# Kernel optimization log

Hardware: AMD Instinct MI355X
Metric: run time of the kernel (lower is better)

The kernel has to match this reference:

```python
import jax, jax.numpy as jnp
import numpy as np

N = 6
DT = 0.02
EPS = 1e-6
_R, _C = np.tril_indices(N)  # row-major lower-triangle order, matches the torch double loop


def _mlp(x, W1, b1, W2, b2, W3, b3):
    h = jax.nn.softplus(x @ W1 + b1)
    h = jax.nn.softplus(h @ W2 + b2)
    return h @ W3 + b3


def _trig(q):
    # interleaved [cos q0, sin q0, cos q1, sin q1, ...]
    return jnp.stack([jnp.cos(q), jnp.sin(q)], axis=-1).reshape(q.shape[:-1] + (2 * N,))


def _mass_single(q, pL):
    # q: (6,) -> M: (6,6)
    y = _mlp(_trig(q), *pL)  # (21,)
    L = jnp.zeros((N, N), y.dtype).at[_R, _C].set(y)
    return L @ L.T + EPS * jnp.eye(N, dtype=y.dtype)


def _mass_batched(q, pL):
    y = _mlp(_trig(q), *pL)  # (B,21)
    L = jnp.zeros((q.shape[0], N, N), y.dtype).at[:, _R, _C].set(y)
    return jnp.einsum('bik,bjk->bij', L, L) + EPS * jnp.eye(N, dtype=y.dtype)


def _pot_batched(q, pV):
    return _mlp(_trig(q), *pV)[:, 0]  # (B,)


def _get_acc(q, qdot, a, pL, pV):
    M = _mass_batched(q, pL)                                   # (B,6,6)
    # per-sample Jacobian dM[i,j]/dq[k] -> (B,6,6,6)
    dM_dq = jax.vmap(jax.jacfwd(lambda qq: _mass_single(qq, pL)))(q)
    # torch: term_1[b,i,j,l] = sum_k M[b,l,k] * dM[b,j,k]/dq[b,i]
    term1 = jnp.einsum('blk,bjki->bijl', M, dM_dq)
    dM = term1 + term1.swapaxes(2, 3)
    c = (jnp.einsum('bjik,bk,bj->bi', dM, qdot, qdot)
         - 0.5 * jnp.einsum('bikj,bk,bj->bi', dM, qdot, qdot))
    # faithful to torch.cholesky_inverse(M): inverse of tril(M) @ tril(M)^T
    Linv = jnp.linalg.inv(jnp.tril(M))
    Minv = Linv.swapaxes(-1, -2) @ Linv
    dV_dq = jax.grad(lambda qq: _pot_batched(qq, pV).sum())(q)  # (B,6)
    return jnp.einsum('bij,bj->bi', Minv, a - c - dV_dq)


def _derivs(s, a, pL, pV):
    q, qdot = s[:, :N], s[:, N:]
    qddot = _get_acc(q, qdot, a, pL, pV)
    return jnp.concatenate([qdot, qddot], axis=1)


def _rk2(s, a, pL, pV):
    alpha = 2.0 / 3.0
    k1 = _derivs(s, a, pL, pV)
    k2 = _derivs(s + alpha * DT * k1, a, pL, pV)
    return s + DT * ((1.0 - 1.0 / (2.0 * alpha)) * k1 + (1.0 / (2.0 * alpha)) * k2)


def setup_inputs() -> dict:
    key = jax.random.key(0)
    ks = jax.random.split(key, 16)
    B = 32768
    def lin(kw, kb, fin, fout):
        s = 1.0 / np.sqrt(fin)
        return (jax.random.uniform(kw, (fin, fout), jnp.float32, -s, s),
                jax.random.uniform(kb, (fout,), jnp.float32, -s, s))
    W1L, b1L = lin(ks[0], ks[1], 12, 128)
    W2L, b2L = lin(ks[2], ks[3], 128, 128)
    W3L, b3L = lin(ks[4], ks[5], 128, 21)
    W1V, b1V = lin(ks[6], ks[7], 12, 128)
    W2V, b2V = lin(ks[8], ks[9], 128, 128)
    W3V, b3V = lin(ks[10], ks[11], 128, 1)
    o = jax.random.normal(ks[12], (B, 18), jnp.float32)
    a = jax.random.normal(ks[13], (B, 6), jnp.float32)
    return {"o": o, "a": a,
            "W1L": W1L, "b1L": b1L, "W2L": W2L, "b2L": b2L, "W3L": W3L, "b3L": b3L,
            "W1V": W1V, "b1V": b1V, "W2V": W2V, "b2V": b2V, "W3V": W3V, "b3V": b3V}


def reference(o, a, W1L, b1L, W2L, b2L, W3L, b3L, W1V, b1V, W2V, b2V, W3V, b3V):
    pL = (W1L, b1L, W2L, b2L, W3L, b3L)
    pV = (W1V, b1V, W2V, b2V, W3V, b3V)
    s = o[:, :2 * N]
    s_next = _rk2(s, a, pL, pV)
    return jnp.concatenate([s_next, o[:, 2 * N:]], axis=1)
```

## Files before the change

### kernel.cpp

```cpp
#include <hip/hip_runtime.h>

#define SMP 64
#define NW 8
#define NT (NW*64)
#define SLC 16

constexpr float DTc  = 0.02f;
constexpr float ADc  = (2.0f/3.0f)*0.02f;
constexpr float EPSc = 1e-6f;

#define FQ   0
#define FQD  6
#define FL   12
#define FM   33
#define FU   69
#define FP   75
#define FR   81
#define FDY  87
#define FDV  108
#define FGV  114
#define FGL  126
#define FC1  138
#define FKQ  144
#define SSTR 151

#define HS 129


__device__ __forceinline__ float softplusf(float z) {
    return fmaxf(z, 0.0f) + __logf(1.0f + __expf(-fabsf(z)));
}
__device__ __forceinline__ float sigmoidf_(float z) {
    float t = __expf(-fabsf(z));
    float r = 1.0f / (1.0f + t);
    return z >= 0.0f ? r : t * r;
}

__global__ void prep_kernel(const float* __restrict__ W1L, const float* __restrict__ W1V,
                            float* __restrict__ ws) {
    int idx = blockIdx.x*256 + threadIdx.x;
    if (idx < 1536) {
        int n = idx / 12, d = idx % 12;
        ws[idx] = W1L[d*128 + n];
    } else if (idx < 3072) {
        int j = idx - 1536;
        int m = j / 12, d = j % 12;
        ws[idx] = W1V[d*128 + m];
    }
}

__launch_bounds__(NT, 2)
__global__ void lnn_kernel(
    const float* __restrict__ o,   const float* __restrict__ aIn,
    const float* __restrict__ b1L, const float* __restrict__ W2L,
    const float* __restrict__ b2L, const float* __restrict__ W3L,
    const float* __restrict__ b3L,
    const float* __restrict__ b1V, const float* __restrict__ W2V,
    const float* __restrict__ b2V, const float* __restrict__ W3V,
    const float* __restrict__ W1LT, const float* __restrict__ W1VT,
    float* __restrict__ out)
{
    __shared__ float H1[SMP*HS];
    __shared__ float HVs[SMP*HS];
    __shared__ float G[SMP*HS];
    __shared__ float S[SMP*SSTR];

    const int tid  = threadIdx.x;
    const int lane = tid & 63;
    const int wv   = __builtin_amdgcn_readfirstlane(tid >> 6);
    const int gs   = blockIdx.x * SMP + lane;
    const int n0   = __builtin_amdgcn_readfirstlane(wv * SLC);
    float* Sl    = &S[lane*SSTR];
    float* Hrow1 = &H1[lane*HS];
    float* HrowV = &HVs[lane*HS];
    float* HrowG = &G[lane*HS];

    constexpr int TRW[21] = {0,1,1,2,2,2,3,3,3,3,4,4,4,4,4,5,5,5,5,5,5};
    constexpr int TCW[21] = {0,0,1,0,1,2,0,1,2,3,0,1,2,3,4,0,1,2,3,4,5};

    float qd[6], tt[12];

    for (int stage = 0; stage < 2; ++stage) {
        {
            float qv[6];
            if (stage == 0) {
                #pragma unroll
                for (int i = 0; i < 6; ++i) { qv[i] = o[gs*18+i]; qd[i] = o[gs*18+6+i]; }
                if (wv == 0) {
                    #pragma unroll
                    for (int i = 0; i < 6; ++i) { Sl[FQ+i] = qv[i]; Sl[FQD+i] = qd[i]; }
                }
            } else {
                #pragma unroll
                for (int i = 0; i < 6; ++i) { qv[i] = Sl[FQ+i]; qd[i] = Sl[FQD+i]; }
            }
            #pragma unroll
            for (int i = 0; i < 6; ++i) { tt[2*i] = cosf(qv[i]); tt[2*i+1] = sinf(qv[i]); }
        }
        if (wv == 1) {
            #pragma unroll
            for (int k = 0; k < 21; ++k) Sl[FL+k] = b3L[k];
        } else if (wv == 2) {
            #pragma unroll
            for (int k = 0; k < 21; ++k) Sl[FDY+k] = 0.0f;
        } else if (wv == 3) {
            #pragma unroll
            for (int d = 0; d < 12; ++d) { Sl[FGV+d] = 0.0f; Sl[FGL+d] = 0.0f; }
        }
        #pragma unroll
        for (int j = 0; j < SLC; ++j) {
            int m = n0 + j;
            const float4* wL = (const float4*)&W1LT[m*12];
            float4 la = wL[0], lb = wL[1], lc = wL[2];
            float zL = b1L[m]
                + tt[0]*la.x + tt[1]*la.y + tt[2] *la.z + tt[3] *la.w
                + tt[4]*lb.x + tt[5]*lb.y + tt[6] *lb.z + tt[7] *lb.w
                + tt[8]*lc.x + tt[9]*lc.y + tt[10]*lc.z + tt[11]*lc.w;
            Hrow1[m] = softplusf(zL);
            const float4* wV = (const float4*)&W1VT[m*12];
            float4 va = wV[0], vb = wV[1], vc = wV[2];
            float zV = b1V[m]
                + tt[0]*va.x + tt[1]*va.y + tt[2] *va.z + tt[3] *va.w
                + tt[4]*vb.x + tt[5]*vb.y + tt[6] *vb.z + tt[7] *vb.w
                + tt[8]*vc.x + tt[9]*vc.y + tt[10]*vc.z + tt[11]*vc.w;
            HrowV[m] = softplusf(zV);
        }
        __syncthreads();

        float sg2reg[SLC];
        {
            float accL[SLC], accV[SLC];
            #pragma unroll
            for (int j = 0; j < SLC; ++j) { accL[j] = b2L[n0+j]; accV[j] = b2V[n0+j]; }
            for (int m8 = 0; m8 < 128; m8 += 8) {
                float h1r[8], hvr[8];
                #pragma unroll
                for (int t = 0; t < 8; ++t) { h1r[t] = Hrow1[m8+t]; hvr[t] = HrowV[m8+t]; }
                #pragma unroll
                for (int t = 0; t < 8; ++t) {
                    const float4* w4 = (const float4*)&W2L[(m8+t)*128 + n0];
                    #pragma unroll
                    for (int g = 0; g < 4; ++g) {
                        float4 w = w4[g];
                        accL[4*g+0] += h1r[t]*w.x; accL[4*g+1] += h1r[t]*w.y;
                        accL[4*g+2] += h1r[t]*w.z; accL[4*g+3] += h1r[t]*w.w;
                    }
                    const float4* v4 = (const float4*)&W2V[(m8+t)*128 + n0];
                    #pragma unroll
                    for (int g = 0; g < 4; ++g) {
                        float4 v = v4[g];
                        accV[4*g+0] += hvr[t]*v.x; accV[4*g+1] += hvr[t]*v.y;
                        accV[4*g+2] += hvr[t]*v.z; accV[4*g+3] += hvr[t]*v.w;
                    }
                }
            }
            float yp[21];
            #pragma unroll
            for (int k = 0; k < 21; ++k) yp[k] = 0.0f;
            #pragma unroll
            for (int j = 0; j < SLC; ++j) {
                int n = n0 + j;
                HrowG[n] = sigmoidf_(accV[j]) * W3V[n];
                sg2reg[j] = sigmoidf_(accL[j]);
                float h2 = softplusf(accL[j]);
                const float* wr = &W3L[n*21];
                #pragma unroll
                for (int k = 0; k < 21; ++k) yp[k] += h2 * wr[k];
            }
            #pragma unroll
            for (int k = 0; k < 21; ++k) atomicAdd(&Sl[FL+k], yp[k]);
        }
        __syncthreads();

        {
            float g1v[SLC];
            #pragma unroll
            for (int j = 0; j < SLC; ++j) g1v[j] = 0.0f;
            for (int nn = 0; nn < 128; nn += 8) {
                float gr[8];
                #pragma unroll
                for (int t = 0; t < 8; ++t) gr[t] = HrowG[nn+t];
                #pragma unroll
                for (int j = 0; j < SLC; ++j) {
                    const float4* w4 = (const float4*)&W2V[(n0+j)*128 + nn];
                    float4 a = w4[0], b = w4[1];
                    g1v[j] += gr[0]*a.x + gr[1]*a.y + gr[2]*a.z + gr[3]*a.w
                            + gr[4]*b.x + gr[5]*b.y + gr[6]*b.z + gr[7]*b.w;
                }
            }
            float gtv[12];
            #pragma unroll
            for (int d = 0; d < 12; ++d) gtv[d] = 0.0f;
            #pragma unroll
            for (int j = 0; j < SLC; ++j) {
                float g1h = g1v[j] * (1.0f - __expf(-HrowV[n0+j]));
                const float4* w4 = (const float4*)&W1VT[(n0+j)*12];
                float4 wa = w4[0], wb = w4[1], wc = w4[2];
                gtv[0] += g1h*wa.x; gtv[1] += g1h*wa.y; gtv[2]  += g1h*wa.z; gtv[3]  += g1h*wa.w;
                gtv[4] += g1h*wb.x; gtv[5] += g1h*wb.y; gtv[6]  += g1h*wb.z; gtv[7]  += g1h*wb.w;
                gtv[8] += g1h*wc.x; gtv[9] += g1h*wc.y; gtv[10] += g1h*wc.z; gtv[11] += g1h*wc.w;
            }
            #pragma unroll
            for (int d = 0; d < 12; ++d) atomicAdd(&Sl[FGV+d], gtv[d]);
        }
        __syncthreads();

        {
            float dtv[12];
            #pragma unroll
            for (int i = 0; i < 6; ++i) { dtv[2*i] = -tt[2*i+1]*qd[i]; dtv[2*i+1] = tt[2*i]*qd[i]; }
            #pragma unroll
            for (int j = 0; j < SLC; ++j) {
                int m = n0 + j;
                const float4* w4 = (const float4*)&W1LT[m*12];
                float4 wa = w4[0], wb = w4[1], wc = w4[2];
                float dz1 = dtv[0]*wa.x + dtv[1]*wa.y + dtv[2] *wa.z + dtv[3] *wa.w
                          + dtv[4]*wb.x + dtv[5]*wb.y + dtv[6] *wb.z + dtv[7] *wb.w
                          + dtv[8]*wc.x + dtv[9]*wc.y + dtv[10]*wc.z + dtv[11]*wc.w;
                float s1 = 1.0f - __expf(-Hrow1[m]);
                HrowV[m] = s1 * dz1;
            }
            if (wv == 0) {
                float Lv[21];
                #pragma unroll
                for (int t = 0; t < 21; ++t) Lv[t] = Sl[FL+t];
                #pragma unroll
                for (int i = 0; i < 6; ++i) {
                    #pragma unroll
                    for (int jj = 0; jj <= i; ++jj) {
                        float s = 0.0f;
                        #pragma unroll
                        for (int k = 0; k <= jj; ++k)
                            s += Lv[(i*(i+1))/2 + k] * Lv[(jj*(jj+1))/2 + k];
                        if (i == jj) s += EPSc;
                        Sl[FM + i*6 + jj] = s;
                        Sl[FM + jj*6 + i] = s;
                    }
                }
                float um[6];
                #pragma unroll
                for (int i = 0; i < 6; ++i) {
                    float s = 0.0f;
                    #pragma unroll
                    for (int jj = 0; jj < 6; ++jj) s += Sl[FM + i*6 + jj] * qd[jj];
                    um[i] = s; Sl[FU+i] = s;
                }
                float pv[6], rv[6];
                #pragma unroll
                for (int i = 0; i < 6; ++i) { pv[i] = 0.0f; rv[i] = 0.0f; }
                #pragma unroll
                for (int t = 0; t < 21; ++t) {
                    pv[TCW[t]] += Lv[t] * qd[TRW[t]];
                    rv[TCW[t]] += Lv[t] * um[TRW[t]];
                }
                #pragma unroll
                for (int i = 0; i < 6; ++i) { Sl[FP+i] = pv[i]; Sl[FR+i] = rv[i]; }
            } else if (wv == 1) {
                #pragma unroll
                for (int i = 0; i < 6; ++i)
                    Sl[FDV+i] = -tt[2*i+1]*Sl[FGV+2*i] + tt[2*i]*Sl[FGV+2*i+1];
            }
        }
        __syncthreads();

        {
            float dz2[SLC];
            #pragma unroll
            for (int j = 0; j < SLC; ++j) dz2[j] = 0.0f;
            for (int m8 = 0; m8 < 128; m8 += 8) {
                float dr[8];
                #pragma unroll
                for (int t = 0; t < 8; ++t) dr[t] = HrowV[m8+t];
                #pragma unroll
                for (int t = 0; t < 8; ++t) {
                    const float4* w4 = (const float4*)&W2L[(m8+t)*128 + n0];
                    #pragma unroll
                    for (int g = 0; g < 4; ++g) {
                        float4 w = w4[g];
                        dz2[4*g+0] += dr[t]*w.x; dz2[4*g+1] += dr[t]*w.y;
                        dz2[4*g+2] += dr[t]*w.z; dz2[4*g+3] += dr[t]*w.w;
                    }
                }
            }
            float dyp[21];
            #pragma unroll
            for (int k = 0; k < 21; ++k) dyp[k] = 0.0f;
            #pragma unroll
            for (int j = 0; j < SLC; ++j) {
                float dh2 = sg2reg[j] * dz2[j];
                const float* wr = &W3L[(n0+j)*21];
                #pragma unroll
                for (int k = 0; k < 21; ++k) dyp[k] += dh2 * wr[k];
            }
            #pragma unroll
            for (int k = 0; k < 21; ++k) atomicAdd(&Sl[FDY+k], dyp[k]);
            float gy[21];
            {
                float uu[6], pp[6], rr[6];
                #pragma unroll
                for (int i = 0; i < 6; ++i) { uu[i]=Sl[FU+i]; pp[i]=Sl[FP+i]; rr[i]=Sl[FR+i]; }
                #pragma unroll
                for (int t = 0; t < 21; ++t)
                    gy[t] = uu[TRW[t]]*pp[TCW[t]] + qd[TRW[t]]*rr[TCW[t]];
            }
            #pragma unroll
            for (int j = 0; j < SLC; ++j) {
                const float* wr = &W3L[(n0+j)*21];
                float gh2 = 0.0f;
                #pragma unroll
                for (int k = 0; k < 21; ++k) gh2 += wr[k] * gy[k];
                HrowG[n0+j] = sg2reg[j] * gh2;
            }
        }
        __syncthreads();

        {
            float gh1[SLC];
            #pragma unroll
            for (int j = 0; j < SLC; ++j) gh1[j] = 0.0f;
            for (int nn = 0; nn < 128; nn += 8) {
                float gr[8];
                #pragma unroll
                for (int t = 0; t < 8; ++t) gr[t] = HrowG[nn+t];
                #pragma unroll
                for (int j = 0; j < SLC; ++j) {
                    const float4* w4 = (const float4*)&W2L[(n0+j)*128 + nn];
                    float4 a = w4[0], b = w4[1];
                    gh1[j] += gr[0]*a.x + gr[1]*a.y + gr[2]*a.z + gr[3]*a.w
                            + gr[4]*b.x + gr[5]*b.y + gr[6]*b.z + gr[7]*b.w;
                }
            }
            float gtl[12];
            #pragma unroll
            for (int d = 0; d < 12; ++d) gtl[d] = 0.0f;
            #pragma unroll
            for (int j = 0; j < SLC; ++j) {
                float gz1 = (1.0f - __expf(-Hrow1[n0+j])) * gh1[j];
                const float4* w4 = (const float4*)&W1LT[(n0+j)*12];
                float4 wa = w4[0], wb = w4[1], wc = w4[2];
                gtl[0] += gz1*wa.x; gtl[1] += gz1*wa.y; gtl[2]  += gz1*wa.z; gtl[3]  += gz1*wa.w;
                gtl[4] += gz1*wb.x; gtl[5] += gz1*wb.y; gtl[6]  += gz1*wb.z; gtl[7]  += gz1*wb.w;
                gtl[8] += gz1*wc.x; gtl[9] += gz1*wc.y; gtl[10] += gz1*wc.z; gtl[11] += gz1*wc.w;
            }
            #pragma unroll
            for (int d = 0; d < 12; ++d) atomicAdd(&Sl[FGL+d], gtl[d]);
            if (wv == 1) {
                float Lv[21], dLv[21];
                #pragma unroll
                for (int t = 0; t < 21; ++t) { Lv[t] = Sl[FL+t]; dLv[t] = Sl[FDY+t]; }
                float Bl[21];
                #pragma unroll
                for (int i = 0; i < 6; ++i) {
                    #pragma unroll
                    for (int jj = 0; jj <= i; ++jj) {
                        float s = 0.0f;
                        #pragma unroll
                        for (int k = 0; k <= jj; ++k)
                            s += dLv[(i*(i+1))/2+k]*Lv[(jj*(jj+1))/2+k]
                               + Lv[(i*(i+1))/2+k]*dLv[(jj*(jj+1))/2+k];
                        Bl[(i*(i+1))/2 + jj] = s;
                    }
                }
                float uu[6];
                #pragma unroll
                for (int i = 0; i < 6; ++i) uu[i] = Sl[FU+i];
                float Bq[6], Bu[6];
                #pragma unroll
                for (int i = 0; i < 6; ++i) {
                    float s1 = 0.0f, s2 = 0.0f;
                    #pragma unroll
                    for (int jj = 0; jj < 6; ++jj) {
                        float Bij = (jj <= i) ? Bl[(i*(i+1))/2 + jj] : Bl[(jj*(jj+1))/2 + i];
                        s1 += Bij*qd[jj]; s2 += Bij*uu[jj];
                    }
                    Bq[i] = s1; Bu[i] = s2;
                }
                #pragma unroll
                for (int i = 0; i < 6; ++i) {
                    float s = 0.0f;
                    #pragma unroll
                    for (int jj = 0; jj < 6; ++jj) s += Sl[FM+i*6+jj]*Bq[jj];
                    Sl[FC1+i] = Bu[i] + s;
                }
            }
        }
        __syncthreads();

        if (wv == 0) {
            float rhs[6];
            #pragma unroll
            for (int i = 0; i < 6; ++i) {
                float c2i = 2.0f*(-tt[2*i+1]*Sl[FGL+2*i] + tt[2*i]*Sl[FGL+2*i+1]);
                float c = Sl[FC1+i] - 0.5f*c2i;
                rhs[i] = aIn[gs*6+i] - c - Sl[FDV+i];
            }
            float Li[21];
            #pragma unroll
            for (int j = 0; j < 6; ++j) {
                float x[6];
                x[j] = 1.0f / Sl[FM + j*6 + j];
                #pragma unroll
                for (int i2 = j+1; i2 < 6; ++i2) {
                    float s = 0.0f;
                    #pragma unroll
                    for (int k = j; k < i2; ++k) s += Sl[FM + i2*6 + k]*x[k];
                    x[i2] = -s / Sl[FM + i2*6 + i2];
                }
                #pragma unroll
                for (int i2 = j; i2 < 6; ++i2) Li[(i2*(i2+1))/2 + j] = x[i2];
            }
            float y1[6];
            #pragma unroll
            for (int i = 0; i < 6; ++i) {
                float s = 0.0f;
                #pragma unroll
                for (int j = 0; j <= i; ++j) s += Li[(i*(i+1))/2+j]*rhs[j];
                y1[i] = s;
            }
            float qdd2[6];
            #pragma unroll
            for (int i = 0; i < 6; ++i) {
                float s = 0.0f;
                #pragma unroll
                for (int k = i; k < 6; ++k) s += Li[(k*(k+1))/2+i]*y1[k];
                qdd2[i] = s;
            }
            if (stage == 0) {
                #pragma unroll
                for (int i = 0; i < 6; ++i) {
                    Sl[FKQ+i] = qdd2[i];
                    Sl[FQ+i]  = Sl[FQ+i] + ADc*qd[i];
                    Sl[FQD+i] = qd[i] + ADc*qdd2[i];
                }
            } else {
                #pragma unroll
                for (int i = 0; i < 6; ++i) {
                    float q0 = o[gs*18+i], qd0 = o[gs*18+6+i];
                    out[gs*18+i]    = q0  + DTc*(0.25f*qd0 + 0.75f*qd[i]);
                    out[gs*18+6+i]  = qd0 + DTc*(0.25f*Sl[FKQ+i] + 0.75f*qdd2[i]);
                    out[gs*18+12+i] = o[gs*18+12+i];
                }
            }
        }
        __syncthreads();
    }
}

extern "C" void kernel_launch(void* const* d_in, const int* in_sizes, int n_in,
                              void* d_out, int out_size, void* d_ws, size_t ws_size,
                              hipStream_t stream) {
    const float* o   = (const float*)d_in[0];
    const float* a   = (const float*)d_in[1];
    const float* W1L = (const float*)d_in[2];
    const float* b1L = (const float*)d_in[3];
    const float* W2L = (const float*)d_in[4];
    const float* b2L = (const float*)d_in[5];
    const float* W3L = (const float*)d_in[6];
    const float* b3L = (const float*)d_in[7];
    const float* W1V = (const float*)d_in[8];
    const float* b1V = (const float*)d_in[9];
    const float* W2V = (const float*)d_in[10];
    const float* b2V = (const float*)d_in[11];
    const float* W3V = (const float*)d_in[12];
    float* ws   = (float*)d_ws;
    float* outp = (float*)d_out;

    hipLaunchKernelGGL(prep_kernel, dim3(12), dim3(256), 0, stream, W1L, W1V, ws);
    hipLaunchKernelGGL(lnn_kernel, dim3(32768/SMP), dim3(NT), 0, stream,
        o, a, b1L, W2L, b2L, W3L, b3L, b1V, W2V, b2V, W3V,
        ws, ws + 1536, outp);
}
```

Measured before the change: 608.6 us.

## Fuse L-net layer-2 forward with its tangent pass to share W2L reads

After: 584.4 us. 4.0% less time.

```diff
diff --git a/kernel.cpp b/kernel.cpp
--- a/kernel.cpp
+++ b/kernel.cpp
@@ -127,24 +127,16 @@
         }
         __syncthreads();
 
-        float sg2reg[SLC];
-        {
-            float accL[SLC], accV[SLC];
-            #pragma unroll
-            for (int j = 0; j < SLC; ++j) { accL[j] = b2L[n0+j]; accV[j] = b2V[n0+j]; }
+        {
+            float accV[SLC];
+            #pragma unroll
+            for (int j = 0; j < SLC; ++j) accV[j] = b2V[n0+j];
             for (int m8 = 0; m8 < 128; m8 += 8) {
-                float h1r[8], hvr[8];
-                #pragma unroll
-                for (int t = 0; t < 8; ++t) { h1r[t] = Hrow1[m8+t]; hvr[t] = HrowV[m8+t]; }
+                float hvr[8];
+                #pragma unroll
+                for (int t = 0; t < 8; ++t) hvr[t] = HrowV[m8+t];
                 #pragma unroll
                 for (int t = 0; t < 8; ++t) {
-                    const float4* w4 = (const float4*)&W2L[(m8+t)*128 + n0];
-                    #pragma unroll
-                    for (int g = 0; g < 4; ++g) {
-                        float4 w = w4[g];
-                        accL[4*g+0] += h1r[t]*w.x; accL[4*g+1] += h1r[t]*w.y;
-                        accL[4*g+2] += h1r[t]*w.z; accL[4*g+3] += h1r[t]*w.w;
-                    }
                     const float4* v4 = (const float4*)&W2V[(m8+t)*128 + n0];
                     #pragma unroll
                     for (int g = 0; g < 4; ++g) {
@@ -154,21 +146,11 @@
                     }
                 }
             }
-            float yp[21];
-            #pragma unroll
-            for (int k = 0; k < 21; ++k) yp[k] = 0.0f;
             #pragma unroll
             for (int j = 0; j < SLC; ++j) {
                 int n = n0 + j;
                 HrowG[n] = sigmoidf_(accV[j]) * W3V[n];
-                sg2reg[j] = sigmoidf_(accL[j]);
-                float h2 = softplusf(accL[j]);
-                const float* wr = &W3L[n*21];
-                #pragma unroll
-                for (int k = 0; k < 21; ++k) yp[k] += h2 * wr[k];
-            }
-            #pragma unroll
-            for (int k = 0; k < 21; ++k) atomicAdd(&Sl[FL+k], yp[k]);
+            }
         }
         __syncthreads();
 
@@ -202,10 +184,6 @@
             }
             #pragma unroll
             for (int d = 0; d < 12; ++d) atomicAdd(&Sl[FGV+d], gtv[d]);
-        }
-        __syncthreads();
-
-        {
             float dtv[12];
             #pragma unroll
             for (int i = 0; i < 6; ++i) { dtv[2*i] = -tt[2*i+1]*qd[i]; dtv[2*i+1] = tt[2*i]*qd[i]; }
@@ -220,80 +198,102 @@
                 float s1 = 1.0f - __expf(-Hrow1[m]);
                 HrowV[m] = s1 * dz1;
             }
-            if (wv == 0) {
-                float Lv[21];
-                #pragma unroll
-                for (int t = 0; t < 21; ++t) Lv[t] = Sl[FL+t];
-                #pragma unroll
-                for (int i = 0; i < 6; ++i) {
-                    #pragma unroll
-                    for (int jj = 0; jj <= i; ++jj) {
-                        float s = 0.0f;
-                        #pragma unroll
-                        for (int k = 0; k <= jj; ++k)
-                            s += Lv[(i*(i+1))/2 + k] * Lv[(jj*(jj+1))/2 + k];
-                        if (i == jj) s += EPSc;
-                        Sl[FM + i*6 + jj] = s;
-                        Sl[FM + jj*6 + i] = s;
-                    }
-                }
-                float um[6];
-                #pragma unroll
-                for (int i = 0; i < 6; ++i) {
-                    float s = 0.0f;
-                    #pragma unroll
-                    for (int jj = 0; jj < 6; ++jj) s += Sl[FM + i*6 + jj] * qd[jj];
-                    um[i] = s; Sl[FU+i] = s;
-                }
-                float pv[6], rv[6];
-                #pragma unroll
-                for (int i = 0; i < 6; ++i) { pv[i] = 0.0f; rv[i] = 0.0f; }
-                #pragma unroll
-                for (int t = 0; t < 21; ++t) {
-                    pv[TCW[t]] += Lv[t] * qd[TRW[t]];
-                    rv[TCW[t]] += Lv[t] * um[TRW[t]];
-                }
-                #pragma unroll
-                for (int i = 0; i < 6; ++i) { Sl[FP+i] = pv[i]; Sl[FR+i] = rv[i]; }
-            } else if (wv == 1) {
-                #pragma unroll
-                for (int i = 0; i < 6; ++i)
-                    Sl[FDV+i] = -tt[2*i+1]*Sl[FGV+2*i] + tt[2*i]*Sl[FGV+2*i+1];
-            }
-        }
-        __syncthreads();
-
-        {
-            float dz2[SLC];
-            #pragma unroll
-            for (int j = 0; j < SLC; ++j) dz2[j] = 0.0f;
+        }
+        __syncthreads();
+
+        {
+            float accL[SLC], dz2[SLC];
+            #pragma unroll
+            for (int j = 0; j < SLC; ++j) { accL[j] = b2L[n0+j]; dz2[j] = 0.0f; }
             for (int m8 = 0; m8 < 128; m8 += 8) {
-                float dr[8];
-                #pragma unroll
-                for (int t = 0; t < 8; ++t) dr[t] = HrowV[m8+t];
+                float h1r[8], dr[8];
+                #pragma unroll
+                for (int t = 0; t < 8; ++t) { h1r[t] = Hrow1[m8+t]; dr[t] = HrowV[m8+t]; }
                 #pragma unroll
                 for (int t = 0; t < 8; ++t) {
                     const float4* w4 = (const float4*)&W2L[(m8+t)*128 + n0];
                     #pragma unroll
                     for (int g = 0; g < 4; ++g) {
                         float4 w = w4[g];
-                        dz2[4*g+0] += dr[t]*w.x; dz2[4*g+1] += dr[t]*w.y;
-                        dz2[4*g+2] += dr[t]*w.z; dz2[4*g+3] += dr[t]*w.w;
+                        accL[4*g+0] += h1r[t]*w.x; accL[4*g+1] += h1r[t]*w.y;
+                        accL[4*g+2] += h1r[t]*w.z; accL[4*g+3] += h1r[t]*w.w;
+                        dz2[4*g+0]  += dr[t]*w.x;  dz2[4*g+1]  += dr[t]*w.y;
+                        dz2[4*g+2]  += dr[t]*w.z;  dz2[4*g+3]  += dr[t]*w.w;
                     }
                 }
             }
+            float yp[21];
+            #pragma unroll
+            for (int k = 0; k < 21; ++k) yp[k] = 0.0f;
+            #pragma unroll
+            for (int j = 0; j < SLC; ++j) {
+                float h2 = softplusf(accL[j]);
+                const float* wr = &W3L[(n0+j)*21];
+                #pragma unroll
+                for (int k = 0; k < 21; ++k) yp[k] += h2 * wr[k];
+            }
+            #pragma unroll
+            for (int k = 0; k < 21; ++k) atomicAdd(&Sl[FL+k], yp[k]);
             float dyp[21];
             #pragma unroll
             for (int k = 0; k < 21; ++k) dyp[k] = 0.0f;
             #pragma unroll
             for (int j = 0; j < SLC; ++j) {
-                float dh2 = sg2reg[j] * dz2[j];
+                float sg2 = sigmoidf_(accL[j]);
+                float dh2 = sg2 * dz2[j];
                 const float* wr = &W3L[(n0+j)*21];
                 #pragma unroll
                 for (int k = 0; k < 21; ++k) dyp[k] += dh2 * wr[k];
+                HrowG[n0+j] = sg2;
             }
             #pragma unroll
             for (int k = 0; k < 21; ++k) atomicAdd(&Sl[FDY+k], dyp[k]);
+        }
+        __syncthreads();
+
+        if (wv == 0) {
+            float Lv[21];
+            #pragma unroll
+            for (int t = 0; t < 21; ++t) Lv[t] = Sl[FL+t];
+            #pragma unroll
+            for (int i = 0; i < 6; ++i) {
+                #pragma unroll
+                for (int jj = 0; jj <= i; ++jj) {
+                    float s = 0.0f;
+                    #pragma unroll
+                    for (int k = 0; k <= jj; ++k)
+                        s += Lv[(i*(i+1))/2 + k] * Lv[(jj*(jj+1))/2 + k];
+                    if (i == jj) s += EPSc;
+                    Sl[FM + i*6 + jj] = s;
+                    Sl[FM + jj*6 + i] = s;
+                }
+            }
+            float um[6];
+            #pragma unroll
+            for (int i = 0; i < 6; ++i) {
+                float s = 0.0f;
+                #pragma unroll
+                for (int jj = 0; jj < 6; ++jj) s += Sl[FM + i*6 + jj] * qd[jj];
+                um[i] = s; Sl[FU+i] = s;
+            }
+            float pv[6], rv[6];
+            #pragma unroll
+            for (int i = 0; i < 6; ++i) { pv[i] = 0.0f; rv[i] = 0.0f; }
+            #pragma unroll
+            for (int t = 0; t < 21; ++t) {
+                pv[TCW[t]] += Lv[t] * qd[TRW[t]];
+                rv[TCW[t]] += Lv[t] * um[TRW[t]];
+            }
+            #pragma unroll
+            for (int i = 0; i < 6; ++i) { Sl[FP+i] = pv[i]; Sl[FR+i] = rv[i]; }
+        } else if (wv == 1) {
+            #pragma unroll
+            for (int i = 0; i < 6; ++i)
+                Sl[FDV+i] = -tt[2*i+1]*Sl[FGV+2*i] + tt[2*i]*Sl[FGV+2*i+1];
+        }
+        __syncthreads();
+
+        {
             float gy[21];
             {
                 float uu[6], pp[6], rr[6];
@@ -309,7 +309,7 @@
                 float gh2 = 0.0f;
                 #pragma unroll
                 for (int k = 0; k < 21; ++k) gh2 += wr[k] * gy[k];
-                HrowG[n0+j] = sg2reg[j] * gh2;
+                HrowG[n0+j] = HrowG[n0+j] * gh2;
             }
         }
         __syncthreads();
```
